# Optimization experiments

Measured on AMD Instinct MI355X. Metric: run time of the kernel, lower is better.

The kernel has to match this reference:

```python
import jax, jax.numpy as jnp
import numpy as np

G = 256        # num_networks
IN_F = 256
OUT_F = 256
N = 262144     # total rows, sum(counts) == N
PAD = 2048     # static per-network padding (>= max count)


def setup_inputs() -> dict:
    key = jax.random.key(0)
    kw, kb, kx = jax.random.split(key, 3)
    scale = 1.0 / np.sqrt(IN_F)
    weight = jax.random.normal(kw, (G, OUT_F, IN_F), jnp.float32) * scale
    bias = jax.random.normal(kb, (G, 1, OUT_F), jnp.float32) * scale
    x = jax.random.normal(kx, (N, IN_F), jnp.float32)
    # irregular per-network row counts summing exactly to N, all < PAD
    rng = np.random.default_rng(0)
    counts = rng.multinomial(N, np.ones(G) / G).astype(np.int32)
    assert counts.max() < PAD and counts.sum() == N
    return {"weight": weight, "bias": bias, "x": x, "counts": jnp.asarray(counts)}


def reference(weight, bias, x, counts):
    # Rows of x are contiguous segments: network g owns rows [offs[g], offs[g]+counts[g]).
    n = x.shape[0]
    offs = jnp.concatenate([jnp.zeros((1,), counts.dtype), jnp.cumsum(counts)])  # [G+1]
    row = jnp.arange(n)
    net_id = jnp.searchsorted(offs[1:], row, side="right")        # [N] network of each row
    rank = row - offs[net_id]                                      # position within segment
    # scatter rows into padded per-network buffer [G, PAD, IN_F]
    buf = jnp.zeros((G, PAD, x.shape[1]), x.dtype).at[net_id, rank].set(x)
    # grouped batched GEMM: y = x_g @ W_g^T + b_g
    y = jnp.einsum("gpi,goi->gpo", buf, weight) + bias             # [G, PAD, OUT_F]
    return y[net_id, rank]                                         # [N, OUT_F]
```

## Files before the change

### kernel.cpp

```cpp
#include <hip/hip_runtime.h>
#include <stdint.h>

#define NG 256
#define KF 256
#define OF 256
#define BM 128
#define BK 64
#define NKT 4
#define NTILES 16
#define NTH 512

typedef unsigned short ushort_t;
using f32x4  = __attribute__((ext_vector_type(4))) float;
using bf16x8 = __attribute__((ext_vector_type(8))) __bf16;
using u16x4  = __attribute__((ext_vector_type(4))) unsigned short;
using u16x8  = __attribute__((ext_vector_type(8))) unsigned short;

__device__ __forceinline__ unsigned short f2bf(float f) {
  unsigned u = __builtin_bit_cast(unsigned, f);
  u += 0x7fffu + ((u >> 16) & 1u);
  return (unsigned short)(u >> 16);
}

__global__ void scan_kernel(const int* __restrict__ counts, int* __restrict__ offs) {
  __shared__ int s[NG];
  int t = threadIdx.x;
  s[t] = counts[t];
  __syncthreads();
  #pragma unroll
  for (int d = 1; d < NG; d <<= 1) {
    int u = (t >= d) ? s[t - d] : 0;
    __syncthreads();
    s[t] += u;
    __syncthreads();
  }
  if (t == 0) offs[0] = 0;
  offs[t + 1] = s[t];
}

__global__ __launch_bounds__(512)
void wconv_kernel(const float* __restrict__ w, unsigned short* __restrict__ img) {
  int tid = blockIdx.x * 512 + threadIdx.x;
  int s  = tid & 7;
  int o  = (tid >> 3) & 255;
  int kc = (tid >> 11) & 3;
  int g  = tid >> 13;
  int k0 = kc * 64 + ((s ^ (o & 7)) << 3);
  const float* src = w + ((size_t)(g * 256 + o) * 256 + k0);
  f32x4 a = *(const f32x4*)src;
  f32x4 b = *(const f32x4*)(src + 4);
  u16x8 r;
  r[0]=f2bf(a[0]); r[1]=f2bf(a[1]); r[2]=f2bf(a[2]); r[3]=f2bf(a[3]);
  r[4]=f2bf(b[0]); r[5]=f2bf(b[1]); r[6]=f2bf(b[2]); r[7]=f2bf(b[3]);
  *(u16x8*)(img + (size_t)tid * 8) = r;
}

template<bool PRECONV>
__global__ __launch_bounds__(NTH)
void gemm_kernel(const float* __restrict__ x,
                 const float* __restrict__ wf32,
                 const unsigned short* __restrict__ wimg,
                 const float* __restrict__ bias,
                 const int* __restrict__ offs,
                 float* __restrict__ out)
{
  __shared__ __align__(16) unsigned short As[BM * BK];
  __shared__ __align__(16) unsigned short Bs[2][OF * BK];

  const int g      = blockIdx.y;
  const int r0     = offs[g];
  const int cnt    = offs[g + 1] - r0;
  const int tstart = blockIdx.x * BM;
  if (tstart >= cnt) return;
  const int mrows = min(BM, cnt - tstart);
  const int row0  = r0 + tstart;

  const int tid  = threadIdx.x;
  const int lane = tid & 63;
  const int wid  = tid >> 6;
  const int wm   = wid >> 2;
  const int wn   = wid & 3;
  const int lrow = lane & 15;
  const int lk   = lane >> 4;

  int  arow_s[4], aq_s[4];
  bool aval[4];
  #pragma unroll
  for (int i = 0; i < 4; ++i) {
    int idx = i * NTH + tid;
    arow_s[i] = idx >> 4;
    aq_s[i]   = idx & 15;
    aval[i]   = arow_s[i] < mrows;
  }

  int arow_f[4], brow_f[4];
  #pragma unroll
  for (int m = 0; m < 4; ++m) arow_f[m] = wm * 64 + m * 16 + lrow;
  #pragma unroll
  for (int n = 0; n < 4; ++n) brow_f[n] = wn * 64 + n * 16 + lrow;

  f32x4 acc[4][4] = {};
  f32x4 aregs[4];
  f32x4 bregs[8];

  auto load_A = [&](int kt) {
    #pragma unroll
    for (int i = 0; i < 4; ++i) {
      if (aval[i])
        aregs[i] = *(const f32x4*)(x + (size_t)(row0 + arow_s[i]) * KF + kt * BK + aq_s[i] * 4);
      else
        aregs[i] = f32x4{0.f, 0.f, 0.f, 0.f};
    }
  };
  auto write_A = [&]() {
    #pragma unroll
    for (int i = 0; i < 4; ++i) {
      int row = arow_s[i], q = aq_s[i];
      int s   = q >> 1;
      int idx = row * 64 + (((s ^ (row & 7)) << 3)) + (q & 1) * 4;
      u16x4 v;
      v[0]=f2bf(aregs[i][0]); v[1]=f2bf(aregs[i][1]);
      v[2]=f2bf(aregs[i][2]); v[3]=f2bf(aregs[i][3]);
      *(u16x4*)&As[idx] = v;
    }
  };
  auto load_B_lds = [&](int kt, int buf) {
    const char* base = (const char*)wimg + ((size_t)(g * 4 + kt) << 15);
    #pragma unroll
    for (int j = 0; j < 4; ++j) {
      int c = wid * 4 + j;
      const void* gsrc = base + c * 1024 + lane * 16;
      void* ldst = (char*)&Bs[buf][0] + c * 1024;
      __builtin_amdgcn_global_load_lds(
          (const __attribute__((address_space(1))) void*)gsrc,
          (__attribute__((address_space(3))) void*)ldst,
          16, 0, 0);
    }
  };
  auto load_B_reg = [&](int kt) {
    #pragma unroll
    for (int i = 0; i < 8; ++i) {
      int idx = i * NTH + tid;
      int ro = idx >> 4, q = idx & 15;
      bregs[i] = *(const f32x4*)(wf32 + (size_t)g * 65536 + (size_t)ro * 256 + kt * BK + q * 4);
    }
  };
  auto write_B_reg = [&](int buf) {
    #pragma unroll
    for (int i = 0; i < 8; ++i) {
      int idx = i * NTH + tid;
      int ro = idx >> 4, q = idx & 15;
      int s  = q >> 1;
      int lidx = ro * 64 + (((s ^ (ro & 7)) << 3)) + (q & 1) * 4;
      u16x4 v;
      v[0]=f2bf(bregs[i][0]); v[1]=f2bf(bregs[i][1]);
      v[2]=f2bf(bregs[i][2]); v[3]=f2bf(bregs[i][3]);
      *(u16x4*)&Bs[buf][lidx] = v;
    }
  };
  auto compute = [&](int buf) {
    #pragma unroll
    for (int kk = 0; kk < 2; ++kk) {
      bf16x8 af[4], bfr[4];
      #pragma unroll
      for (int m = 0; m < 4; ++m) {
        int row = arow_f[m];
        int s   = kk * 4 + lk;
        af[m] = *(const bf16x8*)&As[row * 64 + ((s ^ (row & 7)) << 3)];
      }
      #pragma unroll
      for (int n = 0; n < 4; ++n) {
        int row = brow_f[n];
        int s   = kk * 4 + lk;
        bfr[n] = *(const bf16x8*)&Bs[buf][row * 64 + ((s ^ (row & 7)) << 3)];
      }
      #pragma unroll
      for (int m = 0; m < 4; ++m)
        #pragma unroll
        for (int n = 0; n < 4; ++n)
          acc[m][n] = __builtin_amdgcn_mfma_f32_16x16x32_bf16(af[m], bfr[n], acc[m][n], 0, 0, 0);
    }
  };

  load_A(0);
  if (PRECONV) load_B_lds(0, 0); else load_B_reg(0);
  write_A();
  if (!PRECONV) write_B_reg(0);
  __syncthreads();

  #pragma unroll
  for (int kt = 0; kt < NKT; ++kt) {
    const int  cur  = kt & 1;
    const bool more = (kt + 1) < NKT;
    if (more) {
      load_A(kt + 1);
      if (PRECONV) load_B_lds(kt + 1, cur ^ 1);
      else         load_B_reg(kt + 1);
    }
    compute(cur);
    if (!PRECONV && more) write_B_reg(cur ^ 1);
    if (more) {
      __syncthreads();
      write_A();
      __syncthreads();
    }
  }

  float bb[4];
  #pragma unroll
  for (int n = 0; n < 4; ++n)
    bb[n] = bias[g * OF + wn * 64 + n * 16 + lrow];

  #pragma unroll
  for (int m = 0; m < 4; ++m) {
    int rb = wm * 64 + m * 16 + lk * 4;
    #pragma unroll
    for (int j = 0; j < 4; ++j) {
      int r = rb + j;
      if (r < mrows) {
        float* orow = out + (size_t)(row0 + r) * OF;
        #pragma unroll
        for (int n = 0; n < 4; ++n)
          orow[wn * 64 + n * 16 + lrow] = acc[m][n][j] + bb[n];
      }
    }
  }
}

extern "C" void kernel_launch(void* const* d_in, const int* in_sizes, int n_in,
                              void* d_out, int out_size, void* d_ws, size_t ws_size,
                              hipStream_t stream) {
  const float* weight = (const float*)d_in[0];
  const float* bias   = (const float*)d_in[1];
  const float* x      = (const float*)d_in[2];
  const int*   counts = (const int*)d_in[3];
  float* out = (float*)d_out;

  int* offs = (int*)d_ws;
  unsigned short* wimg = (unsigned short*)((char*)d_ws + 4096);
  const size_t need = 4096 + (size_t)NG * OF * KF * 2;

  scan_kernel<<<1, 256, 0, stream>>>(counts, offs);

  if (ws_size >= need) {
    wconv_kernel<<<(NG * 4 * 256 * 8) / 512, 512, 0, stream>>>(weight, wimg);
    gemm_kernel<true><<<dim3(NTILES, NG), NTH, 0, stream>>>(x, weight, wimg, bias, offs, out);
  } else {
    gemm_kernel<false><<<dim3(NTILES, NG), NTH, 0, stream>>>(x, weight, wimg, bias, offs, out);
  }
}
```

Before: 217.2 us.

## Load A directly into MFMA registers and triple-buffer B with swapped operands

Drops the shared-memory staging of the activation tile. Each wave now owns 16 rows and loads its x fragment straight from global memory into registers, converting it to bf16 there. Weights are tiled with BK=32 into a triple-buffered LDS ring filled via global_load_lds, with manual vmcnt waits so one barrier per k-step replaces two. The MFMA operands are swapped so each lane's output is contiguous, which allows vectorized float4 stores and bias loads. In exchange, every wave rereads the full B tile from LDS (16 reads per k-step), and x is loaded with less coalescing.

```diff
diff --git a/kernel.cpp b/kernel.cpp
--- a/kernel.cpp
+++ b/kernel.cpp
@@ -5,15 +5,13 @@
 #define KF 256
 #define OF 256
 #define BM 128
-#define BK 64
-#define NKT 4
+#define BK 32
+#define NKT 8
 #define NTILES 16
 #define NTH 512
 
-typedef unsigned short ushort_t;
 using f32x4  = __attribute__((ext_vector_type(4))) float;
 using bf16x8 = __attribute__((ext_vector_type(8))) __bf16;
-using u16x4  = __attribute__((ext_vector_type(4))) unsigned short;
 using u16x8  = __attribute__((ext_vector_type(8))) unsigned short;
 
 __device__ __forceinline__ unsigned short f2bf(float f) {
@@ -41,11 +39,11 @@
 __global__ __launch_bounds__(512)
 void wconv_kernel(const float* __restrict__ w, unsigned short* __restrict__ img) {
   int tid = blockIdx.x * 512 + threadIdx.x;
-  int s  = tid & 7;
-  int o  = (tid >> 3) & 255;
-  int kc = (tid >> 11) & 3;
+  int s  = tid & 3;
+  int o  = (tid >> 2) & 255;
+  int kt = (tid >> 10) & 7;
   int g  = tid >> 13;
-  int k0 = kc * 64 + ((s ^ (o & 7)) << 3);
+  int k0 = kt * 32 + ((s ^ (o & 3)) << 3);
   const float* src = w + ((size_t)(g * 256 + o) * 256 + k0);
   f32x4 a = *(const f32x4*)src;
   f32x4 b = *(const f32x4*)(src + 4);
@@ -56,7 +54,7 @@
 }
 
 template<bool PRECONV>
-__global__ __launch_bounds__(NTH)
+__global__ __launch_bounds__(NTH, 4)
 void gemm_kernel(const float* __restrict__ x,
                  const float* __restrict__ wf32,
                  const unsigned short* __restrict__ wimg,
@@ -64,8 +62,7 @@
                  const int* __restrict__ offs,
                  float* __restrict__ out)
 {
-  __shared__ __align__(16) unsigned short As[BM * BK];
-  __shared__ __align__(16) unsigned short Bs[2][OF * BK];
+  __shared__ __align__(16) unsigned short Bs[3][OF * BK];
 
   const int g      = blockIdx.y;
   const int r0     = offs[g];
@@ -77,152 +74,103 @@
 
   const int tid  = threadIdx.x;
   const int lane = tid & 63;
-  const int wid  = tid >> 6;
-  const int wm   = wid >> 2;
-  const int wn   = wid & 3;
+  const int w    = tid >> 6;
   const int lrow = lane & 15;
   const int lk   = lane >> 4;
 
-  int  arow_s[4], aq_s[4];
-  bool aval[4];
-  #pragma unroll
-  for (int i = 0; i < 4; ++i) {
-    int idx = i * NTH + tid;
-    arow_s[i] = idx >> 4;
-    aq_s[i]   = idx & 15;
-    aval[i]   = arow_s[i] < mrows;
-  }
+  const int arow = w * 16 + lrow;
+  const int ar   = row0 + min(arow, mrows - 1);
+  const float* aptr = x + (size_t)ar * KF + lk * 8;
 
-  int arow_f[4], brow_f[4];
-  #pragma unroll
-  for (int m = 0; m < 4; ++m) arow_f[m] = wm * 64 + m * 16 + lrow;
-  #pragma unroll
-  for (int n = 0; n < 4; ++n) brow_f[n] = wn * 64 + n * 16 + lrow;
+  f32x4 areg[2][2];
+  auto issueA = [&](int kt) {
+    const float* p = aptr + kt * BK;
+    areg[kt & 1][0] = *(const f32x4*)(p);
+    areg[kt & 1][1] = *(const f32x4*)(p + 4);
+  };
+  auto mkfrag = [&](int kt) -> bf16x8 {
+    f32x4 lo = areg[kt & 1][0], hi = areg[kt & 1][1];
+    u16x8 r;
+    r[0]=f2bf(lo[0]); r[1]=f2bf(lo[1]); r[2]=f2bf(lo[2]); r[3]=f2bf(lo[3]);
+    r[4]=f2bf(hi[0]); r[5]=f2bf(hi[1]); r[6]=f2bf(hi[2]); r[7]=f2bf(hi[3]);
+    return __builtin_bit_cast(bf16x8, r);
+  };
 
-  f32x4 acc[4][4] = {};
-  f32x4 aregs[4];
-  f32x4 bregs[8];
-
-  auto load_A = [&](int kt) {
+  auto issueB = [&](int kt, int buf) {
+    const char* sb = (const char*)wimg + ((size_t)g << 17) + (size_t)kt * 16384;
     #pragma unroll
-    for (int i = 0; i < 4; ++i) {
-      if (aval[i])
-        aregs[i] = *(const f32x4*)(x + (size_t)(row0 + arow_s[i]) * KF + kt * BK + aq_s[i] * 4);
-      else
-        aregs[i] = f32x4{0.f, 0.f, 0.f, 0.f};
-    }
-  };
-  auto write_A = [&]() {
-    #pragma unroll
-    for (int i = 0; i < 4; ++i) {
-      int row = arow_s[i], q = aq_s[i];
-      int s   = q >> 1;
-      int idx = row * 64 + (((s ^ (row & 7)) << 3)) + (q & 1) * 4;
-      u16x4 v;
-      v[0]=f2bf(aregs[i][0]); v[1]=f2bf(aregs[i][1]);
-      v[2]=f2bf(aregs[i][2]); v[3]=f2bf(aregs[i][3]);
-      *(u16x4*)&As[idx] = v;
-    }
-  };
-  auto load_B_lds = [&](int kt, int buf) {
-    const char* base = (const char*)wimg + ((size_t)(g * 4 + kt) << 15);
-    #pragma unroll
-    for (int j = 0; j < 4; ++j) {
-      int c = wid * 4 + j;
-      const void* gsrc = base + c * 1024 + lane * 16;
-      void* ldst = (char*)&Bs[buf][0] + c * 1024;
+    for (int r = 0; r < 2; ++r) {
+      int c = w * 2 + r;
       __builtin_amdgcn_global_load_lds(
-          (const __attribute__((address_space(1))) void*)gsrc,
-          (__attribute__((address_space(3))) void*)ldst,
+          (const __attribute__((address_space(1))) void*)(sb + c * 1024 + lane * 16),
+          (__attribute__((address_space(3))) void*)((char*)&Bs[buf][0] + c * 1024),
           16, 0, 0);
     }
   };
-  auto load_B_reg = [&](int kt) {
+
+  f32x4 acc[16] = {};
+  const int slot  = lk ^ (lrow & 3);
+  const int bbase = lrow * 32 + slot * 8;
+
+  auto compute = [&](int kt, int buf) {
+    bf16x8 af = mkfrag(kt);
     #pragma unroll
-    for (int i = 0; i < 8; ++i) {
-      int idx = i * NTH + tid;
-      int ro = idx >> 4, q = idx & 15;
-      bregs[i] = *(const f32x4*)(wf32 + (size_t)g * 65536 + (size_t)ro * 256 + kt * BK + q * 4);
-    }
-  };
-  auto write_B_reg = [&](int buf) {
-    #pragma unroll
-    for (int i = 0; i < 8; ++i) {
-      int idx = i * NTH + tid;
-      int ro = idx >> 4, q = idx & 15;
-      int s  = q >> 1;
-      int lidx = ro * 64 + (((s ^ (ro & 7)) << 3)) + (q & 1) * 4;
-      u16x4 v;
-      v[0]=f2bf(bregs[i][0]); v[1]=f2bf(bregs[i][1]);
-      v[2]=f2bf(bregs[i][2]); v[3]=f2bf(bregs[i][3]);
-      *(u16x4*)&Bs[buf][lidx] = v;
-    }
-  };
-  auto compute = [&](int buf) {
-    #pragma unroll
-    for (int kk = 0; kk < 2; ++kk) {
-      bf16x8 af[4], bfr[4];
-      #pragma unroll
-      for (int m = 0; m < 4; ++m) {
-        int row = arow_f[m];
-        int s   = kk * 4 + lk;
-        af[m] = *(const bf16x8*)&As[row * 64 + ((s ^ (row & 7)) << 3)];
-      }
-      #pragma unroll
-      for (int n = 0; n < 4; ++n) {
-        int row = brow_f[n];
-        int s   = kk * 4 + lk;
-        bfr[n] = *(const bf16x8*)&Bs[buf][row * 64 + ((s ^ (row & 7)) << 3)];
-      }
-      #pragma unroll
-      for (int m = 0; m < 4; ++m)
-        #pragma unroll
-        for (int n = 0; n < 4; ++n)
-          acc[m][n] = __builtin_amdgcn_mfma_f32_16x16x32_bf16(af[m], bfr[n], acc[m][n], 0, 0, 0);
+    for (int n = 0; n < 16; ++n) {
+      bf16x8 wf = *(const bf16x8*)&Bs[buf][n * 512 + bbase];
+      acc[n] = __builtin_amdgcn_mfma_f32_16x16x32_bf16(wf, af, acc[n], 0, 0, 0);
     }
   };
 
-  load_A(0);
-  if (PRECONV) load_B_lds(0, 0); else load_B_reg(0);
-  write_A();
-  if (!PRECONV) write_B_reg(0);
-  __syncthreads();
-
-  #pragma unroll
-  for (int kt = 0; kt < NKT; ++kt) {
-    const int  cur  = kt & 1;
-    const bool more = (kt + 1) < NKT;
-    if (more) {
-      load_A(kt + 1);
-      if (PRECONV) load_B_lds(kt + 1, cur ^ 1);
-      else         load_B_reg(kt + 1);
+  if (PRECONV) {
+    issueA(0);
+    issueB(0, 0);
+    issueB(1, 1);
+    #pragma unroll
+    for (int kt = 0; kt < NKT; ++kt) {
+      if (kt < NKT - 1) asm volatile("s_waitcnt vmcnt(2)" ::: "memory");
+      else              asm volatile("s_waitcnt vmcnt(0)" ::: "memory");
+      __builtin_amdgcn_s_barrier();
+      __builtin_amdgcn_sched_barrier(0);
+      if (kt + 1 < NKT) issueA(kt + 1);
+      if (kt + 2 < NKT) issueB(kt + 2, (kt + 2) % 3);
+      __builtin_amdgcn_sched_barrier(0);
+      compute(kt, kt % 3);
     }
-    compute(cur);
-    if (!PRECONV && more) write_B_reg(cur ^ 1);
-    if (more) {
+  } else {
+    #pragma unroll
+    for (int kt = 0; kt < NKT; ++kt) {
+      u16x8 v[2];
+      #pragma unroll
+      for (int r = 0; r < 2; ++r) {
+        int sl = tid + r * 512;
+        int o  = sl >> 2, s = sl & 3;
+        int k  = kt * 32 + ((s ^ (o & 3)) << 3);
+        const float* src = wf32 + ((size_t)(g * 256 + o) * 256 + k);
+        f32x4 a = *(const f32x4*)src;
+        f32x4 b = *(const f32x4*)(src + 4);
+        v[r][0]=f2bf(a[0]); v[r][1]=f2bf(a[1]); v[r][2]=f2bf(a[2]); v[r][3]=f2bf(a[3]);
+        v[r][4]=f2bf(b[0]); v[r][5]=f2bf(b[1]); v[r][6]=f2bf(b[2]); v[r][7]=f2bf(b[3]);
+      }
       __syncthreads();
-      write_A();
+      #pragma unroll
+      for (int r = 0; r < 2; ++r) {
+        int sl = tid + r * 512;
+        *(u16x8*)&Bs[0][sl * 8] = v[r];
+      }
       __syncthreads();
+      issueA(kt);
+      compute(kt, 0);
     }
   }
 
-  float bb[4];
-  #pragma unroll
-  for (int n = 0; n < 4; ++n)
-    bb[n] = bias[g * OF + wn * 64 + n * 16 + lrow];
-
-  #pragma unroll
-  for (int m = 0; m < 4; ++m) {
-    int rb = wm * 64 + m * 16 + lk * 4;
+  if (arow < mrows) {
+    float* orow = out + (size_t)(row0 + arow) * OF;
+    const float* brow = bias + g * OF;
     #pragma unroll
-    for (int j = 0; j < 4; ++j) {
-      int r = rb + j;
-      if (r < mrows) {
-        float* orow = out + (size_t)(row0 + r) * OF;
-        #pragma unroll
-        for (int n = 0; n < 4; ++n)
-          orow[wn * 64 + n * 16 + lrow] = acc[m][n][j] + bb[n];
-      }
+    for (int n = 0; n < 16; ++n) {
+      f32x4 b4 = *(const f32x4*)&brow[n * 16 + lk * 4];
+      f32x4 v  = acc[n] + b4;
+      *(f32x4*)&orow[n * 16 + lk * 4] = v;
     }
   }
 }
@@ -238,12 +186,12 @@
 
   int* offs = (int*)d_ws;
   unsigned short* wimg = (unsigned short*)((char*)d_ws + 4096);
-  const size_t need = 4096 + (size_t)NG * OF * KF * 2;
+  const size_t need = 4096 + (size_t)NG * 8 * 16384;
 
   scan_kernel<<<1, 256, 0, stream>>>(counts, offs);
 
   if (ws_size >= need) {
-    wconv_kernel<<<(NG * 4 * 256 * 8) / 512, 512, 0, stream>>>(weight, wimg);
+    wconv_kernel<<<(NG * 8 * 256 * 4) / 512, 512, 0, stream>>>(weight, wimg);
     gemm_kernel<true><<<dim3(NTILES, NG), NTH, 0, stream>>>(x, weight, wimg, bias, offs, out);
   } else {
     gemm_kernel<false><<<dim3(NTILES, NG), NTH, 0, stream>>>(x, weight, wimg, bias, offs, out);
```

After: 240.5 us. +10.7%, slower.
